# Optimization experiments

Measured on AMD Instinct MI355X. Metric: run time of the kernel, lower is better.

The kernel has to match this reference:

```python
import jax, jax.numpy as jnp
import numpy as np

B, T, D = 4, 4096, 64

def setup_inputs() -> dict:
    key = jax.random.key(0)
    kq, kk, kv = jax.random.split(key, 3)
    Q = jax.random.normal(kq, (B, T, D), dtype=jnp.float32)
    K = jax.random.normal(kk, (B, T, D), dtype=jnp.float32)
    V = jax.random.normal(kv, (B, T, D), dtype=jnp.float32)
    mask = jnp.zeros((B, T, T), dtype=jnp.float32)
    return {"Q": Q, "K": K, "V": V, "mask": mask}

def reference(Q, K, V, mask):
    dk = Q.shape[-1]
    # NOTE: original scales by 1/dk (not 1/sqrt(dk)) -- reproduce faithfully.
    scores = jnp.einsum('btd,bsd->bts', Q, K) * (1.0 / dk)  # [B,T,T]
    scores = scores + mask
    attn = jax.nn.softmax(scores, axis=-1)
    return jnp.einsum('bts,bsd->btd', attn, V)  # [B,T,D]
```

## Files before the change

kernel.cpp:

```cpp
#include <hip/hip_runtime.h>
#include <stdint.h>

#define BB 4
#define TT 4096
#define DD 64
#define KBLK 64

typedef short short8 __attribute__((ext_vector_type(8)));
typedef float f32x4 __attribute__((ext_vector_type(4)));

__device__ __forceinline__ uint16_t f2bf(float x) {
  uint32_t u = __float_as_uint(x);
  u += 0x7FFFu + ((u >> 16) & 1u);
  return (uint16_t)(u >> 16);
}
__device__ __forceinline__ float bf2f(uint16_t h) {
  return __uint_as_float(((uint32_t)h) << 16);
}
__device__ __forceinline__ uint32_t pkbf(float a, float b) {
  return (uint32_t)f2bf(a) | ((uint32_t)f2bf(b) << 16);
}

#define MFMA(a, b, c) __builtin_amdgcn_mfma_f32_16x16x32_bf16((a), (b), (c), 0, 0, 0)

__global__ __launch_bounds__(256) void prep_kernel(
    const float* __restrict__ Q, const float* __restrict__ K, const float* __restrict__ V,
    uint16_t* __restrict__ Qh, uint16_t* __restrict__ Ql,
    uint16_t* __restrict__ Kh, uint16_t* __restrict__ Kl,
    uint16_t* __restrict__ Vh, uint16_t* __restrict__ Vl) {
  __shared__ float vt[64][65];
  const int blk = blockIdx.x;
  const int b = blk >> 6;
  const int r0 = (blk & 63) << 6;
  const int t = threadIdx.x;
  const size_t base = ((size_t)b * TT + r0) * DD;
  for (int i = t; i < 64 * 64; i += 256) {
    float q = Q[base + i] * 0.015625f;
    uint16_t h = f2bf(q);
    Qh[base + i] = h;
    Ql[base + i] = f2bf(q - bf2f(h));
    float k = K[base + i];
    h = f2bf(k);
    Kh[base + i] = h;
    Kl[base + i] = f2bf(k - bf2f(h));
    int r = i >> 6, c = i & 63;
    vt[r][c] = V[base + i];
  }
  __syncthreads();
  for (int i = t; i < 64 * 64; i += 256) {
    int d = i >> 6, c = i & 63;
    float v = vt[c][d];
    uint16_t h = f2bf(v);
    size_t o = ((size_t)b * DD + d) * TT + r0 + c;
    Vh[o] = h;
    Vl[o] = f2bf(v - bf2f(h));
  }
}

template <int NSEG, int NW>
__global__ __launch_bounds__(NW * 64, 4) void attn_kernel(
    const float* __restrict__ mask, float* __restrict__ out,
    float* __restrict__ Op, float* __restrict__ Mp, float* __restrict__ Lp,
    const uint16_t* __restrict__ Qh, const uint16_t* __restrict__ Ql,
    const uint16_t* __restrict__ Kh, const uint16_t* __restrict__ Kl,
    const uint16_t* __restrict__ Vh, const uint16_t* __restrict__ Vl) {
  constexpr int RPB = NW * 16;
  constexpr int PBH = (TT / RPB) / 2;
  constexpr int SEGLEN = TT / NSEG;
  constexpr int NIT = SEGLEN / KBLK;

  __shared__ uint16_t Kh_s[64][72], Kl_s[64][72];
  __shared__ uint16_t Vh_s[64][72], Vl_s[64][72];
  __shared__ uint16_t Ph_s[NW][16][72], Pl_s[NW][16][72];

  const int bid = blockIdx.x;
  const int xcd = bid & 7;
  const int b = xcd >> 1;
  const int u = bid >> 3;
  const int rbl = (u % PBH) * 2 + (xcd & 1);
  const int seg = u / PBH;
  const int q0 = rbl * RPB;
  const int t = threadIdx.x;
  const int w = t >> 6;
  const int l = t & 63;
  const int lr = l & 15;
  const int lq = l >> 4;
  const int qrow = q0 + w * 16;
  const int sb = seg * SEGLEN;

  const uint16_t* qhp = Qh + ((size_t)b * TT + qrow + lr) * DD + lq * 8;
  const uint16_t* qlp = Ql + ((size_t)b * TT + qrow + lr) * DD + lq * 8;
  short8 qh[2], ql[2];
  qh[0] = *(const short8*)(qhp);
  qh[1] = *(const short8*)(qhp + 32);
  ql[0] = *(const short8*)(qlp);
  ql[1] = *(const short8*)(qlp + 32);

  f32x4 o[4];
  float mrow = -1e30f, lrow = 0.f;
#pragma unroll
  for (int dt = 0; dt < 4; ++dt) o[dt] = (f32x4){0.f, 0.f, 0.f, 0.f};

  const float* mprow = mask + ((size_t)b * TT + qrow + lr) * TT + sb + lq * 4;

  f32x4 mk[4];
#pragma unroll
  for (int tt = 0; tt < 4; ++tt)
    mk[tt] = __builtin_nontemporal_load((const f32x4*)(mprow + tt * 16));

  const size_t kvb = (size_t)b * TT * DD;
  const size_t vtb = (size_t)b * DD * TT;

  for (int it = 0; it < NIT; ++it) {
    const int s0 = sb + it * KBLK;
    __syncthreads();
    for (int i = t; i < 512; i += NW * 64) {
      const int row = i >> 3, c = i & 7;
      const size_t ko = kvb + (size_t)(s0 + row) * DD + c * 8;
      *(short8*)&Kh_s[row][c * 8] = *(const short8*)(Kh + ko);
      *(short8*)&Kl_s[row][c * 8] = *(const short8*)(Kl + ko);
      const size_t vo = vtb + (size_t)row * TT + s0 + c * 8;
      *(short8*)&Vh_s[row][c * 8] = *(const short8*)(Vh + vo);
      *(short8*)&Vl_s[row][c * 8] = *(const short8*)(Vl + vo);
    }
    __syncthreads();

    f32x4 mk2[4];
    if (it + 1 < NIT) {
#pragma unroll
      for (int tt = 0; tt < 4; ++tt)
        mk2[tt] = __builtin_nontemporal_load((const f32x4*)(mprow + (it + 1) * KBLK + tt * 16));
    } else {
#pragma unroll
      for (int tt = 0; tt < 4; ++tt) mk2[tt] = (f32x4){0.f, 0.f, 0.f, 0.f};
    }

    f32x4 s[4];
#pragma unroll
    for (int tt = 0; tt < 4; ++tt) {
      f32x4 acc = (f32x4){0.f, 0.f, 0.f, 0.f};
#pragma unroll
      for (int c = 0; c < 2; ++c) {
        const short8 bh = *(const short8*)&Kh_s[tt * 16 + lr][c * 32 + lq * 8];
        const short8 bl = *(const short8*)&Kl_s[tt * 16 + lr][c * 32 + lq * 8];
        acc = MFMA(bh, qh[c], acc);
        acc = MFMA(bl, qh[c], acc);
        acc = MFMA(bh, ql[c], acc);
      }
      s[tt] = acc;
    }
#pragma unroll
    for (int tt = 0; tt < 4; ++tt) s[tt] += mk[tt];

    float cm = fmaxf(fmaxf(fmaxf(s[0][0], s[0][1]), fmaxf(s[0][2], s[0][3])),
                     fmaxf(fmaxf(s[1][0], s[1][1]), fmaxf(s[1][2], s[1][3])));
    cm = fmaxf(cm, fmaxf(fmaxf(fmaxf(s[2][0], s[2][1]), fmaxf(s[2][2], s[2][3])),
                         fmaxf(fmaxf(s[3][0], s[3][1]), fmaxf(s[3][2], s[3][3]))));
    cm = fmaxf(cm, __shfl_xor(cm, 16));
    cm = fmaxf(cm, __shfl_xor(cm, 32));
    if (!__all(cm <= mrow + 8.0f)) {
      const float mn = fmaxf(mrow, cm);
      const float scl = __expf(mrow - mn);
      mrow = mn;
      lrow *= scl;
      float sj[4];
#pragma unroll
      for (int j = 0; j < 4; ++j) sj[j] = __shfl(scl, lq * 4 + j);
#pragma unroll
      for (int dt = 0; dt < 4; ++dt)
#pragma unroll
        for (int j = 0; j < 4; ++j) o[dt][j] *= sj[j];
    }
#pragma unroll
    for (int tt = 0; tt < 4; ++tt)
#pragma unroll
      for (int j = 0; j < 4; ++j) s[tt][j] = __expf(s[tt][j] - mrow);
    float rs = ((s[0][0] + s[0][1]) + (s[0][2] + s[0][3])) +
               ((s[1][0] + s[1][1]) + (s[1][2] + s[1][3])) +
               ((s[2][0] + s[2][1]) + (s[2][2] + s[2][3])) +
               ((s[3][0] + s[3][1]) + (s[3][2] + s[3][3]));
    rs += __shfl_xor(rs, 16);
    rs += __shfl_xor(rs, 32);
    lrow += rs;

#pragma unroll
    for (int tt = 0; tt < 4; ++tt) {
      float e0 = s[tt][0], e1 = s[tt][1], e2 = s[tt][2], e3 = s[tt][3];
      *(uint32_t*)&Ph_s[w][lr][tt * 16 + lq * 4] = pkbf(e0, e1);
      *(uint32_t*)&Ph_s[w][lr][tt * 16 + lq * 4 + 2] = pkbf(e2, e3);
      float r0 = e0 - bf2f(f2bf(e0)), r1 = e1 - bf2f(f2bf(e1));
      float r2 = e2 - bf2f(f2bf(e2)), r3 = e3 - bf2f(f2bf(e3));
      *(uint32_t*)&Pl_s[w][lr][tt * 16 + lq * 4] = pkbf(r0, r1);
      *(uint32_t*)&Pl_s[w][lr][tt * 16 + lq * 4 + 2] = pkbf(r2, r3);
    }

#pragma unroll
    for (int c = 0; c < 2; ++c) {
      const short8 ph = *(const short8*)&Ph_s[w][lr][c * 32 + lq * 8];
      const short8 pl = *(const short8*)&Pl_s[w][lr][c * 32 + lq * 8];
#pragma unroll
      for (int dt = 0; dt < 4; ++dt) {
        const short8 vh = *(const short8*)&Vh_s[dt * 16 + lr][c * 32 + lq * 8];
        const short8 vl = *(const short8*)&Vl_s[dt * 16 + lr][c * 32 + lq * 8];
        o[dt] = MFMA(ph, vh, o[dt]);
        o[dt] = MFMA(pl, vh, o[dt]);
        o[dt] = MFMA(ph, vl, o[dt]);
      }
    }

#pragma unroll
    for (int tt = 0; tt < 4; ++tt) mk[tt] = mk2[tt];
  }

  if constexpr (NSEG == 1) {
    const float linv = 1.0f / lrow;
#pragma unroll
    for (int j = 0; j < 4; ++j) {
      const float inv = __shfl(linv, lq * 4 + j);
      const size_t ob = ((size_t)b * TT + qrow + lq * 4 + j) * DD + lr;
#pragma unroll
      for (int dt = 0; dt < 4; ++dt) out[ob + dt * 16] = o[dt][j] * inv;
    }
  } else {
    const int grow = b * TT + qrow;
#pragma unroll
    for (int j = 0; j < 4; ++j) {
      const size_t r = (size_t)seg * (BB * TT) + grow + lq * 4 + j;
#pragma unroll
      for (int dt = 0; dt < 4; ++dt) Op[r * 64 + dt * 16 + lr] = o[dt][j];
    }
    if (lq == 0) {
      const size_t r = (size_t)seg * (BB * TT) + grow + lr;
      Mp[r] = mrow;
      Lp[r] = lrow;
    }
  }
}

__global__ __launch_bounds__(256) void combine_kernel(
    const float* __restrict__ Op, const float* __restrict__ Mp,
    const float* __restrict__ Lp, float* __restrict__ out, int nseg) {
  const int gid = blockIdx.x * 256 + threadIdx.x;
  const int r = gid >> 6, d = gid & 63;
  constexpr int ROWS = BB * TT;
  float m = -3.0e38f;
  for (int s = 0; s < nseg; ++s) m = fmaxf(m, Mp[s * ROWS + r]);
  float num = 0.f, den = 0.f;
  for (int s = 0; s < nseg; ++s) {
    const float e = __expf(Mp[s * ROWS + r] - m);
    den += Lp[s * ROWS + r] * e;
    num += Op[((size_t)s * ROWS + r) * 64 + d] * e;
  }
  out[(size_t)r * 64 + d] = num / den;
}

extern "C" void kernel_launch(void* const* d_in, const int* in_sizes, int n_in,
                              void* d_out, int out_size, void* d_ws, size_t ws_size,
                              hipStream_t stream) {
  const float* Q = (const float*)d_in[0];
  const float* K = (const float*)d_in[1];
  const float* V = (const float*)d_in[2];
  const float* mask = (const float*)d_in[3];
  float* out = (float*)d_out;

  const size_t NE = (size_t)BB * TT * DD;
  const size_t ROWS = (size_t)BB * TT;
  uint16_t* ws = (uint16_t*)d_ws;
  uint16_t* Qh = ws;
  uint16_t* Ql = ws + NE;
  uint16_t* Kh = ws + 2 * NE;
  uint16_t* Kl = ws + 3 * NE;
  uint16_t* Vh = ws + 4 * NE;
  uint16_t* Vl = ws + 5 * NE;

  const size_t bf_bytes = 6 * NE * 2;
  const size_t per_seg = ROWS * 64 * 4 + ROWS * 2 * 4;
  int nseg = (ws_size >= bf_bytes + 4 * per_seg) ? 4
           : (ws_size >= bf_bytes + 2 * per_seg) ? 2 : 1;

  char* pbase = (char*)d_ws + bf_bytes;
  float* Op = (float*)pbase;
  float* Mp = (float*)(pbase + (size_t)nseg * ROWS * 64 * 4);
  float* Lp = Mp + (size_t)nseg * ROWS;

  prep_kernel<<<dim3(256), dim3(256), 0, stream>>>(Q, K, V, Qh, Ql, Kh, Kl, Vh, Vl);

  if (nseg == 4) {
    attn_kernel<4, 8><<<dim3(512), dim3(512), 0, stream>>>(
        mask, out, Op, Mp, Lp, Qh, Ql, Kh, Kl, Vh, Vl);
  } else if (nseg == 2) {
    attn_kernel<2, 8><<<dim3(256), dim3(512), 0, stream>>>(
        mask, out, Op, Mp, Lp, Qh, Ql, Kh, Kl, Vh, Vl);
  } else {
    attn_kernel<1, 4><<<dim3(256), dim3(256), 0, stream>>>(
        mask, out, Op, Mp, Lp, Qh, Ql, Kh, Kl, Vh, Vl);
  }
  if (nseg > 1) {
    combine_kernel<<<dim3((ROWS * 64) / 256), dim3(256), 0, stream>>>(Op, Mp, Lp, out, nseg);
  }
}
```

Before: 400.0 us.

## Double-buffer K/V tiles via direct global-to-LDS loads and register P exchange

Replaces the single-buffered K/V shared tiles with two XOR-swizzled buffers filled by global_load_lds, so the next tile's fetch overlaps the current tile's compute and only one barrier is needed per tile. The P matrix is now moved from the QK output layout to the PV operand layout with lane shuffles instead of a round trip through shared memory. The aim is to hide global load latency and cut LDS traffic and bank conflicts. In exchange it doubles the LDS footprint, which may lower occupancy, adds shuffle work, and requires an even iteration count.

```diff
diff --git a/kernel.cpp b/kernel.cpp
--- a/kernel.cpp
+++ b/kernel.cpp
@@ -8,6 +8,7 @@
 
 typedef short short8 __attribute__((ext_vector_type(8)));
 typedef float f32x4 __attribute__((ext_vector_type(4)));
+typedef uint32_t u32x4 __attribute__((ext_vector_type(4)));
 
 __device__ __forceinline__ uint16_t f2bf(float x) {
   uint32_t u = __float_as_uint(x);
@@ -57,6 +58,131 @@
   }
 }
 
+
+#define STAGE(KH, KL, VH, VL, S0)                                              \
+  do {                                                                         \
+    _Pragma("unroll") for (int c = t; c < 512; c += NW * 64) {                 \
+      const int cb8 = (c & ~63) * 8;           \
+      const int row = c >> 3;                                                  \
+      const int ssl = (c & 7) ^ (row & 7);                                     \
+      const size_t ksrc = kvb + (size_t)((S0) + row) * DD + ssl * 8;           \
+      const size_t vsrc = vtb + (size_t)row * TT + (S0) + ssl * 8;             \
+      __builtin_amdgcn_global_load_lds(Kh + ksrc, &KH[cb8], 16, 0, 0);         \
+      __builtin_amdgcn_global_load_lds(Kl + ksrc, &KL[cb8], 16, 0, 0);         \
+      __builtin_amdgcn_global_load_lds(Vh + vsrc, &VH[cb8], 16, 0, 0);         \
+      __builtin_amdgcn_global_load_lds(Vl + vsrc, &VL[cb8], 16, 0, 0);         \
+    }                                                                          \
+  } while (0)
+
+#define LOADMASK(MK, TILE)                                                     \
+  do {                                                                         \
+    _Pragma("unroll") for (int q_ = 0; q_ < 4; ++q_)                           \
+        MK[q_] = __builtin_nontemporal_load(                                   \
+            (const f32x4*)(mprow + (size_t)(TILE) * KBLK + q_ * 16));          \
+  } while (0)
+
+#define LOADMASK_Z(MK)                                                         \
+  do {                                                                         \
+    _Pragma("unroll") for (int q_ = 0; q_ < 4; ++q_)                           \
+        MK[q_] = (f32x4){0.f, 0.f, 0.f, 0.f};                                  \
+  } while (0)
+
+#define PACK(TT_, HA, HB, LA, LB)                                              \
+  {                                                                            \
+    const float a0 = s_[TT_][0], a1 = s_[TT_][1];                              \
+    const float a2 = s_[TT_][2], a3 = s_[TT_][3];                              \
+    const uint16_t h0 = f2bf(a0), h1 = f2bf(a1);                               \
+    const uint16_t h2 = f2bf(a2), h3 = f2bf(a3);                               \
+    HA = (uint32_t)h0 | ((uint32_t)h1 << 16);                                  \
+    HB = (uint32_t)h2 | ((uint32_t)h3 << 16);                                  \
+    LA = pkbf(a0 - bf2f(h0), a1 - bf2f(h1));                                   \
+    LB = pkbf(a2 - bf2f(h2), a3 - bf2f(h3));                                   \
+  }
+
+#define XCHG(W, SA0, SB0, SA1, SB1)                                            \
+  {                                                                            \
+    const uint32_t A0 = __shfl(SA0, src0), A1 = __shfl(SB0, src0);             \
+    const uint32_t B0 = __shfl(SA1, src0), B1 = __shfl(SB1, src0);             \
+    const uint32_t A2 = __shfl(SA0, src1), A3 = __shfl(SB0, src1);             \
+    const uint32_t B2 = __shfl(SA1, src1), B3 = __shfl(SB1, src1);             \
+    W = (u32x4){hi2 ? B0 : A0, hi2 ? B1 : A1, hi2 ? B2 : A2, hi2 ? B3 : A3};   \
+  }
+
+#define COMPUTE(KH, KL, VH, VL, MK)                                            \
+  do {                                                                         \
+    f32x4 s_[4];                                                               \
+    _Pragma("unroll") for (int tt = 0; tt < 4; ++tt) {                         \
+      f32x4 acc = (f32x4){0.f, 0.f, 0.f, 0.f};                                 \
+      const short8 bh0 = *(const short8*)&KH[(tt * 16 + lr) * 64 + sw0 * 8];   \
+      const short8 bl0 = *(const short8*)&KL[(tt * 16 + lr) * 64 + sw0 * 8];   \
+      acc = MFMA(bh0, qh[0], acc);                                             \
+      acc = MFMA(bl0, qh[0], acc);                                             \
+      acc = MFMA(bh0, ql[0], acc);                                             \
+      const short8 bh1 = *(const short8*)&KH[(tt * 16 + lr) * 64 + sw1 * 8];   \
+      const short8 bl1 = *(const short8*)&KL[(tt * 16 + lr) * 64 + sw1 * 8];   \
+      acc = MFMA(bh1, qh[1], acc);                                             \
+      acc = MFMA(bl1, qh[1], acc);                                             \
+      acc = MFMA(bh1, ql[1], acc);                                             \
+      s_[tt] = acc + MK[tt];                                                   \
+    }                                                                          \
+    float cm = fmaxf(fmaxf(fmaxf(s_[0][0], s_[0][1]), fmaxf(s_[0][2], s_[0][3])), \
+                     fmaxf(fmaxf(s_[1][0], s_[1][1]), fmaxf(s_[1][2], s_[1][3]))); \
+    cm = fmaxf(cm, fmaxf(fmaxf(fmaxf(s_[2][0], s_[2][1]), fmaxf(s_[2][2], s_[2][3])), \
+                         fmaxf(fmaxf(s_[3][0], s_[3][1]), fmaxf(s_[3][2], s_[3][3])))); \
+    cm = fmaxf(cm, __shfl_xor(cm, 16));                                        \
+    cm = fmaxf(cm, __shfl_xor(cm, 32));                                        \
+    if (!__all(cm <= mrow + 8.0f)) {                      \
+      const float mn = fmaxf(mrow, cm);                                        \
+      const float scl = __expf(mrow - mn);                                     \
+      mrow = mn;                                                               \
+      lrow *= scl;                                                             \
+      float sj0 = __shfl(scl, lq * 4 + 0), sj1 = __shfl(scl, lq * 4 + 1);      \
+      float sj2 = __shfl(scl, lq * 4 + 2), sj3 = __shfl(scl, lq * 4 + 3);      \
+      _Pragma("unroll") for (int dt = 0; dt < 4; ++dt) {                       \
+        o[dt][0] *= sj0; o[dt][1] *= sj1; o[dt][2] *= sj2; o[dt][3] *= sj3;    \
+      }                                                                        \
+    }                                                                          \
+    _Pragma("unroll") for (int tt = 0; tt < 4; ++tt)                           \
+        _Pragma("unroll") for (int j = 0; j < 4; ++j)                          \
+            s_[tt][j] = __expf(s_[tt][j] - mrow);                              \
+    float rs = ((s_[0][0] + s_[0][1]) + (s_[0][2] + s_[0][3])) +               \
+               ((s_[1][0] + s_[1][1]) + (s_[1][2] + s_[1][3])) +               \
+               ((s_[2][0] + s_[2][1]) + (s_[2][2] + s_[2][3])) +               \
+               ((s_[3][0] + s_[3][1]) + (s_[3][2] + s_[3][3]));                \
+    rs += __shfl_xor(rs, 16);                                                  \
+    rs += __shfl_xor(rs, 32);                                                  \
+    lrow += rs;                                                                \
+    uint32_t H0a, H0b, L0a, L0b, H1a, H1b, L1a, L1b;                           \
+    uint32_t H2a, H2b, L2a, L2b, H3a, H3b, L3a, L3b;                           \
+    PACK(0, H0a, H0b, L0a, L0b)                                                \
+    PACK(1, H1a, H1b, L1a, L1b)                                                \
+    PACK(2, H2a, H2b, L2a, L2b)                                                \
+    PACK(3, H3a, H3b, L3a, L3b)                                                \
+    u32x4 wh0, wl0, wh1, wl1;                                                  \
+    XCHG(wh0, H0a, H0b, H1a, H1b)                                              \
+    XCHG(wl0, L0a, L0b, L1a, L1b)                                              \
+    XCHG(wh1, H2a, H2b, H3a, H3b)                                              \
+    XCHG(wl1, L2a, L2b, L3a, L3b)                                              \
+    const short8 ph0 = __builtin_bit_cast(short8, wh0);                        \
+    const short8 pl0 = __builtin_bit_cast(short8, wl0);                        \
+    const short8 ph1 = __builtin_bit_cast(short8, wh1);                        \
+    const short8 pl1 = __builtin_bit_cast(short8, wl1);                        \
+    _Pragma("unroll") for (int dt = 0; dt < 4; ++dt) {                         \
+      const short8 vh = *(const short8*)&VH[(dt * 16 + lr) * 64 + sw0 * 8];    \
+      const short8 vl = *(const short8*)&VL[(dt * 16 + lr) * 64 + sw0 * 8];    \
+      o[dt] = MFMA(ph0, vh, o[dt]);                                            \
+      o[dt] = MFMA(pl0, vh, o[dt]);                                            \
+      o[dt] = MFMA(ph0, vl, o[dt]);                                            \
+    }                                                                          \
+    _Pragma("unroll") for (int dt = 0; dt < 4; ++dt) {                         \
+      const short8 vh = *(const short8*)&VH[(dt * 16 + lr) * 64 + sw1 * 8];    \
+      const short8 vl = *(const short8*)&VL[(dt * 16 + lr) * 64 + sw1 * 8];    \
+      o[dt] = MFMA(ph1, vh, o[dt]);                                            \
+      o[dt] = MFMA(pl1, vh, o[dt]);                                            \
+      o[dt] = MFMA(ph1, vl, o[dt]);                                            \
+    }                                                                          \
+  } while (0)
+
 template <int NSEG, int NW>
 __global__ __launch_bounds__(NW * 64, 4) void attn_kernel(
     const float* __restrict__ mask, float* __restrict__ out,
@@ -68,10 +194,10 @@
   constexpr int PBH = (TT / RPB) / 2;
   constexpr int SEGLEN = TT / NSEG;
   constexpr int NIT = SEGLEN / KBLK;
-
-  __shared__ uint16_t Kh_s[64][72], Kl_s[64][72];
-  __shared__ uint16_t Vh_s[64][72], Vl_s[64][72];
-  __shared__ uint16_t Ph_s[NW][16][72], Pl_s[NW][16][72];
+  static_assert((NIT & 1) == 0, "NIT must be even for 2x-unrolled dbuf");
+
+  __shared__ uint16_t KhA[4096], KlA[4096], VhA[4096], VlA[4096];
+  __shared__ uint16_t KhB[4096], KlB[4096], VhB[4096], VlB[4096];
 
   const int bid = blockIdx.x;
   const int xcd = bid & 7;
@@ -88,6 +214,12 @@
   const int qrow = q0 + w * 16;
   const int sb = seg * SEGLEN;
 
+  const int sw0 = lq ^ (lr & 7);
+  const int sw1 = sw0 ^ 4;
+  const int src0 = lr + (((2 * lq) & 3) << 4);
+  const int src1 = lr + (((2 * lq + 1) & 3) << 4);
+  const int hi2 = lq >> 1;
+
   const uint16_t* qhp = Qh + ((size_t)b * TT + qrow + lr) * DD + lq * 8;
   const uint16_t* qlp = Ql + ((size_t)b * TT + qrow + lr) * DD + lq * 8;
   short8 qh[2], ql[2];
@@ -102,114 +234,28 @@
   for (int dt = 0; dt < 4; ++dt) o[dt] = (f32x4){0.f, 0.f, 0.f, 0.f};
 
   const float* mprow = mask + ((size_t)b * TT + qrow + lr) * TT + sb + lq * 4;
-
-  f32x4 mk[4];
-#pragma unroll
-  for (int tt = 0; tt < 4; ++tt)
-    mk[tt] = __builtin_nontemporal_load((const f32x4*)(mprow + tt * 16));
-
   const size_t kvb = (size_t)b * TT * DD;
   const size_t vtb = (size_t)b * DD * TT;
 
-  for (int it = 0; it < NIT; ++it) {
-    const int s0 = sb + it * KBLK;
+  f32x4 mk0[4], mk1[4];
+  STAGE(KhA, KlA, VhA, VlA, sb);
+  LOADMASK(mk0, 0);
+  __syncthreads();
+
+  for (int itp = 0; itp < NIT / 2; ++itp) {
+    const int it0 = 2 * itp;
+    STAGE(KhB, KlB, VhB, VlB, sb + (it0 + 1) * KBLK);
+    LOADMASK(mk1, it0 + 1);
+    COMPUTE(KhA, KlA, VhA, VlA, mk0);
     __syncthreads();
-    for (int i = t; i < 512; i += NW * 64) {
-      const int row = i >> 3, c = i & 7;
-      const size_t ko = kvb + (size_t)(s0 + row) * DD + c * 8;
-      *(short8*)&Kh_s[row][c * 8] = *(const short8*)(Kh + ko);
-      *(short8*)&Kl_s[row][c * 8] = *(const short8*)(Kl + ko);
-      const size_t vo = vtb + (size_t)row * TT + s0 + c * 8;
-      *(short8*)&Vh_s[row][c * 8] = *(const short8*)(Vh + vo);
-      *(short8*)&Vl_s[row][c * 8] = *(const short8*)(Vl + vo);
+    if (it0 + 2 < NIT) {
+      STAGE(KhA, KlA, VhA, VlA, sb + (it0 + 2) * KBLK);
+      LOADMASK(mk0, it0 + 2);
+    } else {
+      LOADMASK_Z(mk0);
     }
+    COMPUTE(KhB, KlB, VhB, VlB, mk1);
     __syncthreads();
-
-    f32x4 mk2[4];
-    if (it + 1 < NIT) {
-#pragma unroll
-      for (int tt = 0; tt < 4; ++tt)
-        mk2[tt] = __builtin_nontemporal_load((const f32x4*)(mprow + (it + 1) * KBLK + tt * 16));
-    } else {
-#pragma unroll
-      for (int tt = 0; tt < 4; ++tt) mk2[tt] = (f32x4){0.f, 0.f, 0.f, 0.f};
-    }
-
-    f32x4 s[4];
-#pragma unroll
-    for (int tt = 0; tt < 4; ++tt) {
-      f32x4 acc = (f32x4){0.f, 0.f, 0.f, 0.f};
-#pragma unroll
-      for (int c = 0; c < 2; ++c) {
-        const short8 bh = *(const short8*)&Kh_s[tt * 16 + lr][c * 32 + lq * 8];
-        const short8 bl = *(const short8*)&Kl_s[tt * 16 + lr][c * 32 + lq * 8];
-        acc = MFMA(bh, qh[c], acc);
-        acc = MFMA(bl, qh[c], acc);
-        acc = MFMA(bh, ql[c], acc);
-      }
-      s[tt] = acc;
-    }
-#pragma unroll
-    for (int tt = 0; tt < 4; ++tt) s[tt] += mk[tt];
-
-    float cm = fmaxf(fmaxf(fmaxf(s[0][0], s[0][1]), fmaxf(s[0][2], s[0][3])),
-                     fmaxf(fmaxf(s[1][0], s[1][1]), fmaxf(s[1][2], s[1][3])));
-    cm = fmaxf(cm, fmaxf(fmaxf(fmaxf(s[2][0], s[2][1]), fmaxf(s[2][2], s[2][3])),
-                         fmaxf(fmaxf(s[3][0], s[3][1]), fmaxf(s[3][2], s[3][3]))));
-    cm = fmaxf(cm, __shfl_xor(cm, 16));
-    cm = fmaxf(cm, __shfl_xor(cm, 32));
-    if (!__all(cm <= mrow + 8.0f)) {
-      const float mn = fmaxf(mrow, cm);
-      const float scl = __expf(mrow - mn);
-      mrow = mn;
-      lrow *= scl;
-      float sj[4];
-#pragma unroll
-      for (int j = 0; j < 4; ++j) sj[j] = __shfl(scl, lq * 4 + j);
-#pragma unroll
-      for (int dt = 0; dt < 4; ++dt)
-#pragma unroll
-        for (int j = 0; j < 4; ++j) o[dt][j] *= sj[j];
-    }
-#pragma unroll
-    for (int tt = 0; tt < 4; ++tt)
-#pragma unroll
-      for (int j = 0; j < 4; ++j) s[tt][j] = __expf(s[tt][j] - mrow);
-    float rs = ((s[0][0] + s[0][1]) + (s[0][2] + s[0][3])) +
-               ((s[1][0] + s[1][1]) + (s[1][2] + s[1][3])) +
-               ((s[2][0] + s[2][1]) + (s[2][2] + s[2][3])) +
-               ((s[3][0] + s[3][1]) + (s[3][2] + s[3][3]));
-    rs += __shfl_xor(rs, 16);
-    rs += __shfl_xor(rs, 32);
-    lrow += rs;
-
-#pragma unroll
-    for (int tt = 0; tt < 4; ++tt) {
-      float e0 = s[tt][0], e1 = s[tt][1], e2 = s[tt][2], e3 = s[tt][3];
-      *(uint32_t*)&Ph_s[w][lr][tt * 16 + lq * 4] = pkbf(e0, e1);
-      *(uint32_t*)&Ph_s[w][lr][tt * 16 + lq * 4 + 2] = pkbf(e2, e3);
-      float r0 = e0 - bf2f(f2bf(e0)), r1 = e1 - bf2f(f2bf(e1));
-      float r2 = e2 - bf2f(f2bf(e2)), r3 = e3 - bf2f(f2bf(e3));
-      *(uint32_t*)&Pl_s[w][lr][tt * 16 + lq * 4] = pkbf(r0, r1);
-      *(uint32_t*)&Pl_s[w][lr][tt * 16 + lq * 4 + 2] = pkbf(r2, r3);
-    }
-
-#pragma unroll
-    for (int c = 0; c < 2; ++c) {
-      const short8 ph = *(const short8*)&Ph_s[w][lr][c * 32 + lq * 8];
-      const short8 pl = *(const short8*)&Pl_s[w][lr][c * 32 + lq * 8];
-#pragma unroll
-      for (int dt = 0; dt < 4; ++dt) {
-        const short8 vh = *(const short8*)&Vh_s[dt * 16 + lr][c * 32 + lq * 8];
-        const short8 vl = *(const short8*)&Vl_s[dt * 16 + lr][c * 32 + lq * 8];
-        o[dt] = MFMA(ph, vh, o[dt]);
-        o[dt] = MFMA(pl, vh, o[dt]);
-        o[dt] = MFMA(ph, vl, o[dt]);
-      }
-    }
-
-#pragma unroll
-    for (int tt = 0; tt < 4; ++tt) mk[tt] = mk2[tt];
   }
 
   if constexpr (NSEG == 1) {
```

Measured after the change: 404.6 us. No clear change (+1.1%).
